# Optimization experiments

Measured on AMD Instinct MI355X. Metric: run time of the kernel, lower is better.

The kernel has to match this reference:

```python
import jax, jax.numpy as jnp
import numpy as np

VOCAB, EMBED, HIDDEN, OUT = 32000, 300, 512, 7


def setup_inputs() -> dict:
    key = jax.random.key(0)
    ks = jax.random.split(key, 8)
    tokens = jax.random.randint(ks[0], (256, 512), 0, VOCAB, dtype=jnp.int32)
    # embedding table (padding_idx=0 row zeroed inside reference)
    emb = jax.random.normal(ks[1], (VOCAB, EMBED), dtype=jnp.float32)
    # xavier-uniform-like init for recurrent weights
    lim_ih = float(np.sqrt(6.0 / (EMBED + 4 * HIDDEN)))
    lim_hh = float(np.sqrt(6.0 / (HIDDEN + 4 * HIDDEN)))
    W_ih = jax.random.uniform(ks[2], (4 * HIDDEN, EMBED), jnp.float32, -lim_ih, lim_ih)
    W_hh = jax.random.uniform(ks[3], (4 * HIDDEN, HIDDEN), jnp.float32, -lim_hh, lim_hh)
    b_ih = jax.random.uniform(ks[4], (4 * HIDDEN,), jnp.float32, -0.05, 0.05)
    b_hh = jax.random.uniform(ks[5], (4 * HIDDEN,), jnp.float32, -0.05, 0.05)
    lim_fc = float(np.sqrt(1.0 / HIDDEN))
    W_fc = jax.random.uniform(ks[6], (OUT, HIDDEN), jnp.float32, -lim_fc, lim_fc)
    b_fc = jax.random.uniform(ks[7], (OUT,), jnp.float32, -lim_fc, lim_fc)
    return {"tokens": tokens, "emb": emb, "W_ih": W_ih, "b_ih": b_ih,
            "W_hh": W_hh, "b_hh": b_hh, "W_fc": W_fc, "b_fc": b_fc}


def reference(tokens, emb, W_ih, b_ih, W_hh, b_hh, W_fc, b_fc):
    B, S = tokens.shape
    H = W_hh.shape[1]
    # padding_idx=0: row 0 of the embedding table is zero
    emb = emb.at[0].set(0.0)
    x_emb = emb[tokens]  # [B, S, E]
    # precompute input projections for all timesteps in one GEMM
    gx = jnp.einsum('bse,ge->bsg', x_emb, W_ih) + b_ih  # [B, S, 4H]
    gx_t = jnp.moveaxis(gx, 1, 0)  # [S, B, 4H]

    def step(carry, g_x):
        h, c = carry
        gates = g_x + h @ W_hh.T + b_hh  # [B, 4H]
        i_g, f_g, g_g, o_g = jnp.split(gates, 4, axis=1)
        i = jax.nn.sigmoid(i_g)
        f = jax.nn.sigmoid(f_g)
        g = jnp.tanh(g_g)
        o = jax.nn.sigmoid(o_g)
        c_next = f * c + i * g
        h_next = o * jnp.tanh(c_next)
        return (h_next, c_next), None

    h0 = jnp.zeros((B, H), dtype=x_emb.dtype)
    c0 = jnp.zeros((B, H), dtype=x_emb.dtype)
    (h_T, _), _ = jax.lax.scan(step, (h0, c0), gx_t)
    # dropout is identity in eval mode
    logits = h_T @ W_fc.T + b_fc  # [B, OUT]
    return logits
```

## Files before the change

### kernel.cpp

```cpp
#include <hip/hip_runtime.h>
#include <hip/hip_bf16.h>


typedef unsigned short ushort_t;
typedef unsigned long long u64_t;
typedef __bf16 bf16x8 __attribute__((ext_vector_type(8)));
typedef unsigned short u16x8v __attribute__((ext_vector_type(8)));
typedef float f32x4 __attribute__((ext_vector_type(4)));

#define U_STRIDE 840
#define HOFF 320
#define SCR_S 36

__device__ __forceinline__ float sigmoidf_(float x) { return 1.0f / (1.0f + __expf(-x)); }
__device__ __forceinline__ float tanhf_(float x)    { return 1.0f - 2.0f / (__expf(2.0f * x) + 1.0f); }

__device__ __forceinline__ ushort_t f2bf(float f) {
    unsigned u = __builtin_bit_cast(unsigned, f);
    unsigned r = (u + 0x7FFFu + ((u >> 16) & 1u)) >> 16;
    return (ushort_t)r;
}
__device__ __forceinline__ float bf2f(ushort_t u) {
    unsigned v = ((unsigned)u) << 16;
    return __builtin_bit_cast(float, v);
}

__device__ __forceinline__ u64_t g_load64(const u64_t* p) {
    return __hip_atomic_load(p, __ATOMIC_RELAXED, __HIP_MEMORY_SCOPE_AGENT);
}
__device__ __forceinline__ void g_store64(u64_t* p, u64_t v) {
    __hip_atomic_store(p, v, __ATOMIC_RELAXED, __HIP_MEMORY_SCOPE_AGENT);
}
__device__ __forceinline__ int g_load_flag(const int* p) {
    return __hip_atomic_load(p, __ATOMIC_RELAXED, __HIP_MEMORY_SCOPE_AGENT);
}
__device__ __forceinline__ void g_store_flag(int* p, int v) {
    __hip_atomic_store(p, v, __ATOMIC_RELAXED, __HIP_MEMORY_SCOPE_AGENT);
}

__global__ __launch_bounds__(256, 1)
void lstm_fused_kernel(const int* __restrict__ tokens,
                       const float* __restrict__ emb,
                       const float* __restrict__ Wih,
                       const float* __restrict__ bih,
                       const float* __restrict__ Whh,
                       const float* __restrict__ bhh,
                       const float* __restrict__ Wfc,
                       const float* __restrict__ bfc,
                       float* __restrict__ out,
                       int* __restrict__ flags,
                       ushort_t* __restrict__ hbuf)
{
    __shared__ ushort_t u_lds[16 * U_STRIDE];
    __shared__ ushort_t h_scr[16 * SCR_S];

    const int tid = threadIdx.x;
    const int bid = blockIdx.x;
    const int g   = bid & 15;
    const int ib  = bid >> 4;
    const int Bg0 = g * 16;
    const int U0  = ib * 32;
    const int lane = tid & 63;
    const int wv   = tid >> 6;
    const int lm   = lane & 15;
    const int q    = lane >> 4;

    bf16x8 aih[2][10];
    bf16x8 ahh[2][16];
#pragma unroll
    for (int m = 0; m < 2; ++m) {
        const int rp   = 32 * wv + 16 * m + lm;
        const int gi   = rp & 3;
        const int up   = rp >> 2;
        const int grow = gi * 512 + U0 + up;
#pragma unroll
        for (int kc = 0; kc < 10; ++kc) {
            u16x8v tmp;
#pragma unroll
            for (int j = 0; j < 8; ++j) {
                int col = 32 * kc + 8 * q + j;
                tmp[j] = (col < 300) ? f2bf(Wih[grow * 300 + col]) : (ushort_t)0;
            }
            aih[m][kc] = __builtin_bit_cast(bf16x8, tmp);
        }
#pragma unroll
        for (int kc = 0; kc < 16; ++kc) {
            u16x8v tmp;
#pragma unroll
            for (int j = 0; j < 8; ++j) {
                int col = 32 * kc + 8 * q + j;
                tmp[j] = f2bf(Whh[grow * 512 + col]);
            }
            ahh[m][kc] = __builtin_bit_cast(bf16x8, tmp);
        }
    }

    float bias[2][4];
#pragma unroll
    for (int m = 0; m < 2; ++m) {
        const int unit = U0 + 8 * wv + 4 * m + q;
#pragma unroll
        for (int j = 0; j < 4; ++j)
            bias[m][j] = bih[j * 512 + unit] + bhh[j * 512 + unit];
    }

    if (tid < 128) {
        int r = tid >> 3;
        int d = tid & 7;
        g_store64((u64_t*)(hbuf + (size_t)(Bg0 + r) * 512 + U0 + 4 * d), 0ull);
    }
    __syncthreads();
    if (tid == 0) g_store_flag(&flags[g * 16 + ib], 1);

    const int* myflag = &flags[g * 16 + (lane & 15)];
    float c0 = 0.0f, c1 = 0.0f;

    const int xr  = tid >> 4;
    const int xln = tid & 15;
    const int xb  = Bg0 + xr;
    int tok_cur = tokens[xb * 512 + 0];
    int tok_nxt = tokens[xb * 512 + 1];
    float2 xp[10];
    {
        const float2* s2 = (const float2*)(emb + (size_t)tok_cur * 300);
#pragma unroll
        for (int k = 0; k < 10; ++k) {
            int i = xln + 16 * k;
            if (i < 150) xp[k] = s2[i];
        }
    }

    for (int t = 0; t < 512; ++t) {
        {
            unsigned int* dstx = (unsigned int*)(u_lds + xr * U_STRIDE);
            const bool tz = (tok_cur != 0);
#pragma unroll
            for (int k = 0; k < 10; ++k) {
                int i = xln + 16 * k;
                unsigned int v = 0u;
                if (tz && i < 150)
                    v = (unsigned int)f2bf(xp[k].x) | ((unsigned int)f2bf(xp[k].y) << 16);
                dstx[i] = v;
            }
        }
        {
            tok_cur = tok_nxt;
            const float2* s2 = (const float2*)(emb + (size_t)tok_cur * 300);
#pragma unroll
            for (int k = 0; k < 10; ++k) {
                int i = xln + 16 * k;
                if (i < 150) xp[k] = s2[i];
            }
            int t2 = (t + 2 < 512) ? (t + 2) : 511;
            tok_nxt = tokens[xb * 512 + t2];
        }
        __syncthreads();

        f32x4 acc0 = {0.f, 0.f, 0.f, 0.f};
        f32x4 acc1 = {0.f, 0.f, 0.f, 0.f};
        const ushort_t* u0 = u_lds + lm * U_STRIDE + 8 * q;
#pragma unroll
        for (int kc = 0; kc < 10; ++kc) {
            bf16x8 b0 = __builtin_bit_cast(bf16x8, *(const u16x8v*)(u0 + 32 * kc));
            acc0 = __builtin_amdgcn_mfma_f32_16x16x32_bf16(aih[0][kc], b0, acc0, 0, 0, 0);
            acc1 = __builtin_amdgcn_mfma_f32_16x16x32_bf16(aih[1][kc], b0, acc1, 0, 0, 0);
        }

        if (wv == 0) {
            const int target = t + 1;
            while (true) {
                int v = g_load_flag(myflag);
                if (__all(v >= target)) break;
                __builtin_amdgcn_s_sleep(1);
            }
            asm volatile("" ::: "memory");
        }
        __syncthreads();

        {
            const int r  = tid >> 4;
            const int ln = tid & 15;
            const u64_t* hsrc = (const u64_t*)(hbuf + (size_t)(t & 1) * (256 * 512)
                                               + (size_t)(Bg0 + r) * 512);
            u64_t* dsth = (u64_t*)(u_lds + r * U_STRIDE + HOFF);
            u64_t tmp[8];
#pragma unroll
            for (int k = 0; k < 8; ++k) tmp[k] = g_load64(hsrc + ln + 16 * k);
#pragma unroll
            for (int k = 0; k < 8; ++k) dsth[ln + 16 * k] = tmp[k];
        }
        __syncthreads();

#pragma unroll
        for (int kc = 0; kc < 16; ++kc) {
            bf16x8 b0 = __builtin_bit_cast(bf16x8, *(const u16x8v*)(u0 + HOFF + 32 * kc));
            acc0 = __builtin_amdgcn_mfma_f32_16x16x32_bf16(ahh[0][kc], b0, acc0, 0, 0, 0);
            acc1 = __builtin_amdgcn_mfma_f32_16x16x32_bf16(ahh[1][kc], b0, acc1, 0, 0, 0);
        }

        {
            {
                float ig = sigmoidf_(acc0.x + bias[0][0]);
                float fg = sigmoidf_(acc0.y + bias[0][1]);
                float gg = tanhf_(acc0.z + bias[0][2]);
                float og = sigmoidf_(acc0.w + bias[0][3]);
                c0 = fg * c0 + ig * gg;
                h_scr[lm * SCR_S + 8 * wv + q] = f2bf(og * tanhf_(c0));
            }
            {
                float ig = sigmoidf_(acc1.x + bias[1][0]);
                float fg = sigmoidf_(acc1.y + bias[1][1]);
                float gg = tanhf_(acc1.z + bias[1][2]);
                float og = sigmoidf_(acc1.w + bias[1][3]);
                c1 = fg * c1 + ig * gg;
                h_scr[lm * SCR_S + 8 * wv + 4 + q] = f2bf(og * tanhf_(c1));
            }
        }
        __syncthreads();

        if (tid < 128) {
            const int r = tid >> 3;
            const int d = tid & 7;
            u64_t v = *(const u64_t*)((const char*)h_scr + r * (SCR_S * 2) + d * 8);
            ushort_t* hdst = hbuf + (size_t)((t + 1) & 1) * (256 * 512);
            g_store64((u64_t*)(hdst + (size_t)(Bg0 + r) * 512 + U0 + 4 * d), v);
        }
        __syncthreads();
        if (tid == 0) g_store_flag(&flags[g * 16 + ib], t + 2);
    }

    if (wv == 0) {
        while (true) {
            int v = g_load_flag(myflag);
            if (__all(v >= 513)) break;
            __builtin_amdgcn_s_sleep(1);
        }
        asm volatile("" ::: "memory");
    }
    __syncthreads();

    {
        const int bb = Bg0 + ib;
        const ushort_t* hrow = hbuf + (size_t)bb * 512;
        u64_t h0 = g_load64((const u64_t*)(hrow + lane * 8));
        u64_t h1 = g_load64((const u64_t*)(hrow + lane * 8 + 4));
        float hv[8];
#pragma unroll
        for (int j = 0; j < 4; ++j) hv[j]     = bf2f((ushort_t)(h0 >> (16 * j)));
#pragma unroll
        for (int j = 0; j < 4; ++j) hv[4 + j] = bf2f((ushort_t)(h1 >> (16 * j)));
#pragma unroll
        for (int oo = 0; oo < 2; ++oo) {
            int o = wv + 4 * oo;
            if (o < 7) {
                f32x4 w0 = *(const f32x4*)(Wfc + o * 512 + lane * 8);
                f32x4 w1 = *(const f32x4*)(Wfc + o * 512 + lane * 8 + 4);
                float s = hv[0] * w0.x + hv[1] * w0.y + hv[2] * w0.z + hv[3] * w0.w
                        + hv[4] * w1.x + hv[5] * w1.y + hv[6] * w1.z + hv[7] * w1.w;
#pragma unroll
                for (int sh = 32; sh >= 1; sh >>= 1) s += __shfl_down(s, sh);
                if (lane == 0)
                    out[bb * 7 + o] = s + bfc[o];
            }
        }
    }
}

extern "C" void kernel_launch(void* const* d_in, const int* in_sizes, int n_in,
                              void* d_out, int out_size, void* d_ws, size_t ws_size,
                              hipStream_t stream) {
    const int* tokens = (const int*)d_in[0];
    const float* emb  = (const float*)d_in[1];
    const float* Wih  = (const float*)d_in[2];
    const float* bih  = (const float*)d_in[3];
    const float* Whh  = (const float*)d_in[4];
    const float* bhh  = (const float*)d_in[5];
    const float* Wfc  = (const float*)d_in[6];
    const float* bfc  = (const float*)d_in[7];

    int* flags      = (int*)d_ws;
    ushort_t* hbuf  = (ushort_t*)((char*)d_ws + 1024);

    lstm_fused_kernel<<<dim3(256), dim3(256), 0, stream>>>(
        tokens, emb, Wih, bih, Whh, bhh, Wfc, bfc,
        (float*)d_out, flags, hbuf);
}
```

Measured before the change: 1.549 ms.

## Overlap hbuf global load with x-embedding MFMA and split accumulators

```diff
diff --git a/kernel.cpp b/kernel.cpp
--- a/kernel.cpp
+++ b/kernel.cpp
@@ -36,6 +36,13 @@
 }
 __device__ __forceinline__ void g_store_flag(int* p, int v) {
     __hip_atomic_store(p, v, __ATOMIC_RELAXED, __HIP_MEMORY_SCOPE_AGENT);
+}
+
+__device__ __forceinline__ void bar_lgkm() {
+    asm volatile("s_waitcnt lgkmcnt(0)\n\ts_barrier" ::: "memory");
+}
+__device__ __forceinline__ void bar_raw() {
+    asm volatile("s_barrier" ::: "memory");
 }
 
 __global__ __launch_bounds__(256, 1)
@@ -114,6 +121,8 @@
 
     const int* myflag = &flags[g * 16 + (lane & 15)];
     float c0 = 0.0f, c1 = 0.0f;
+    int v0 = 0;
+    if (wv == 0) v0 = g_load_flag(myflag);
 
     const int xr  = tid >> 4;
     const int xln = tid & 15;
@@ -131,6 +140,29 @@
     }
 
     for (int t = 0; t < 512; ++t) {
+        if (wv == 0) {
+            const int target = t + 1;
+            if (!__all(v0 >= target)) {
+                while (true) {
+                    int v = g_load_flag(myflag);
+                    if (__all(v >= target)) break;
+                    __builtin_amdgcn_s_sleep(1);
+                }
+            }
+            asm volatile("" ::: "memory");
+        }
+        bar_raw();
+
+        const int hr  = tid >> 4;
+        const int hln = tid & 15;
+        u64_t htmp[8];
+        {
+            const u64_t* hsrc = (const u64_t*)(hbuf + (size_t)(t & 1) * (256 * 512)
+                                               + (size_t)(Bg0 + hr) * 512);
+#pragma unroll
+            for (int k = 0; k < 8; ++k) htmp[k] = g_load64(hsrc + hln + 16 * k);
+        }
+
         {
             unsigned int* dstx = (unsigned int*)(u_lds + xr * U_STRIDE);
             const bool tz = (tok_cur != 0);
@@ -154,69 +186,57 @@
             int t2 = (t + 2 < 512) ? (t + 2) : 511;
             tok_nxt = tokens[xb * 512 + t2];
         }
-        __syncthreads();
-
-        f32x4 acc0 = {0.f, 0.f, 0.f, 0.f};
-        f32x4 acc1 = {0.f, 0.f, 0.f, 0.f};
+        bar_lgkm();
+
+        f32x4 acc[2][4];
+#pragma unroll
+        for (int m = 0; m < 2; ++m)
+#pragma unroll
+            for (int c = 0; c < 4; ++c)
+                acc[m][c] = (f32x4){0.f, 0.f, 0.f, 0.f};
         const ushort_t* u0 = u_lds + lm * U_STRIDE + 8 * q;
 #pragma unroll
         for (int kc = 0; kc < 10; ++kc) {
             bf16x8 b0 = __builtin_bit_cast(bf16x8, *(const u16x8v*)(u0 + 32 * kc));
-            acc0 = __builtin_amdgcn_mfma_f32_16x16x32_bf16(aih[0][kc], b0, acc0, 0, 0, 0);
-            acc1 = __builtin_amdgcn_mfma_f32_16x16x32_bf16(aih[1][kc], b0, acc1, 0, 0, 0);
-        }
-
-        if (wv == 0) {
-            const int target = t + 1;
-            while (true) {
-                int v = g_load_flag(myflag);
-                if (__all(v >= target)) break;
-                __builtin_amdgcn_s_sleep(1);
-            }
-            asm volatile("" ::: "memory");
-        }
-        __syncthreads();
-
-        {
-            const int r  = tid >> 4;
-            const int ln = tid & 15;
-            const u64_t* hsrc = (const u64_t*)(hbuf + (size_t)(t & 1) * (256 * 512)
-                                               + (size_t)(Bg0 + r) * 512);
-            u64_t* dsth = (u64_t*)(u_lds + r * U_STRIDE + HOFF);
-            u64_t tmp[8];
-#pragma unroll
-            for (int k = 0; k < 8; ++k) tmp[k] = g_load64(hsrc + ln + 16 * k);
-#pragma unroll
-            for (int k = 0; k < 8; ++k) dsth[ln + 16 * k] = tmp[k];
-        }
-        __syncthreads();
+            acc[0][kc & 3] = __builtin_amdgcn_mfma_f32_16x16x32_bf16(aih[0][kc], b0, acc[0][kc & 3], 0, 0, 0);
+            acc[1][kc & 3] = __builtin_amdgcn_mfma_f32_16x16x32_bf16(aih[1][kc], b0, acc[1][kc & 3], 0, 0, 0);
+        }
+
+        {
+            u64_t* dsth = (u64_t*)(u_lds + hr * U_STRIDE + HOFF);
+#pragma unroll
+            for (int k = 0; k < 8; ++k) dsth[hln + 16 * k] = htmp[k];
+        }
+        bar_lgkm();
 
 #pragma unroll
         for (int kc = 0; kc < 16; ++kc) {
             bf16x8 b0 = __builtin_bit_cast(bf16x8, *(const u16x8v*)(u0 + HOFF + 32 * kc));
-            acc0 = __builtin_amdgcn_mfma_f32_16x16x32_bf16(ahh[0][kc], b0, acc0, 0, 0, 0);
-            acc1 = __builtin_amdgcn_mfma_f32_16x16x32_bf16(ahh[1][kc], b0, acc1, 0, 0, 0);
+            acc[0][kc & 3] = __builtin_amdgcn_mfma_f32_16x16x32_bf16(ahh[0][kc], b0, acc[0][kc & 3], 0, 0, 0);
+            acc[1][kc & 3] = __builtin_amdgcn_mfma_f32_16x16x32_bf16(ahh[1][kc], b0, acc[1][kc & 3], 0, 0, 0);
         }
 
         {
             {
-                float ig = sigmoidf_(acc0.x + bias[0][0]);
-                float fg = sigmoidf_(acc0.y + bias[0][1]);
-                float gg = tanhf_(acc0.z + bias[0][2]);
-                float og = sigmoidf_(acc0.w + bias[0][3]);
+                f32x4 a = (acc[0][0] + acc[0][1]) + (acc[0][2] + acc[0][3]);
+                float ig = sigmoidf_(a.x + bias[0][0]);
+                float fg = sigmoidf_(a.y + bias[0][1]);
+                float gg = tanhf_(a.z + bias[0][2]);
+                float og = sigmoidf_(a.w + bias[0][3]);
                 c0 = fg * c0 + ig * gg;
                 h_scr[lm * SCR_S + 8 * wv + q] = f2bf(og * tanhf_(c0));
             }
             {
-                float ig = sigmoidf_(acc1.x + bias[1][0]);
-                float fg = sigmoidf_(acc1.y + bias[1][1]);
-                float gg = tanhf_(acc1.z + bias[1][2]);
-                float og = sigmoidf_(acc1.w + bias[1][3]);
+                f32x4 a = (acc[1][0] + acc[1][1]) + (acc[1][2] + acc[1][3]);
+                float ig = sigmoidf_(a.x + bias[1][0]);
+                float fg = sigmoidf_(a.y + bias[1][1]);
+                float gg = tanhf_(a.z + bias[1][2]);
+                float og = sigmoidf_(a.w + bias[1][3]);
                 c1 = fg * c1 + ig * gg;
                 h_scr[lm * SCR_S + 8 * wv + 4 + q] = f2bf(og * tanhf_(c1));
             }
         }
-        __syncthreads();
+        bar_lgkm();
 
         if (tid < 128) {
             const int r = tid >> 3;
@@ -225,8 +245,10 @@
             ushort_t* hdst = hbuf + (size_t)((t + 1) & 1) * (256 * 512);
             g_store64((u64_t*)(hdst + (size_t)(Bg0 + r) * 512 + U0 + 4 * d), v);
         }
-        __syncthreads();
+        if (wv < 2) asm volatile("s_waitcnt vmcnt(0)" ::: "memory");
+        bar_raw();
         if (tid == 0) g_store_flag(&flags[g * 16 + ib], t + 2);
+        if (wv == 0) v0 = g_load_flag(myflag);
     }
 
     if (wv == 0) {
```

After: 1.814 ms. 1.17x slower.
